# Optimization experiments

Measured on AMD Instinct MI355X. Metric: run time of the kernel, lower is better.

Reference implementation:

```python
import jax, jax.numpy as jnp
import numpy as np

B, C, N, M = 4096, 1024, 256, 64
EPS = 1e-8


def _linear_params(key, out_dim, in_dim):
    kw, kb = jax.random.split(key)
    lim = 1.0 / np.sqrt(in_dim)
    W = jax.random.uniform(kw, (out_dim, in_dim), jnp.float32, -lim, lim)
    b = jax.random.uniform(kb, (out_dim,), jnp.float32, -lim, lim)
    return W, b


def setup_inputs() -> dict:
    key = jax.random.key(0)
    ks = jax.random.split(key, 10)
    emb = jax.random.normal(ks[0], (B, C), jnp.float32)
    w_prev = jax.random.uniform(ks[1], (B, N), jnp.float32)
    w_prev = w_prev / jnp.sum(w_prev, axis=1, keepdims=True)  # valid weighting
    memory = jax.random.normal(ks[2], (B, N, M), jnp.float32) * 0.1
    Wk, bk = _linear_params(ks[3], M, C)
    Wbeta, bbeta = _linear_params(ks[4], 1, C)
    Wg, bg = _linear_params(ks[5], 1, C)
    Ws, bs = _linear_params(ks[6], 3, C)
    Wgamma, bgamma = _linear_params(ks[7], 1, C)
    We, be = _linear_params(ks[8], M, C)
    Wa, ba = _linear_params(ks[9], M, C)
    return {
        'embeddings': emb, 'w_prev': w_prev, 'memory': memory,
        'Wk': Wk, 'bk': bk, 'Wbeta': Wbeta, 'bbeta': bbeta,
        'Wg': Wg, 'bg': bg, 'Ws': Ws, 'bs': bs,
        'Wgamma': Wgamma, 'bgamma': bgamma,
        'We': We, 'be': be, 'Wa': Wa, 'ba': ba,
    }


def _forward(embeddings, w_prev, memory, Wk, bk, Wbeta, bbeta, Wg, bg,
             Ws, bs, Wgamma, bgamma, We, be, Wa, ba):
    k = embeddings @ Wk.T + bk                                  # [B, M]
    beta = jax.nn.softplus(embeddings @ Wbeta.T + bbeta)        # [B, 1]
    g = jax.nn.sigmoid(embeddings @ Wg.T + bg)                  # [B, 1]
    s = jax.nn.softmax(embeddings @ Ws.T + bs, axis=1)          # [B, 3]
    gamma = 1.0 + jax.nn.softplus(embeddings @ Wgamma.T + bgamma)  # [B, 1]
    e = jax.nn.sigmoid(embeddings @ We.T + be)                  # [B, M]
    a = embeddings @ Wa.T + ba                                  # [B, M]

    # content addressing: beta-scaled cosine similarity + softmax
    dot = jnp.einsum('bnm,bm->bn', memory, k)                   # [B, N]
    mem_norm = jnp.linalg.norm(memory, axis=-1)                 # [B, N]
    k_norm = jnp.linalg.norm(k, axis=-1, keepdims=True)         # [B, 1]
    cos = dot / (jnp.maximum(mem_norm, EPS) * jnp.maximum(k_norm, EPS))
    w_c = jax.nn.softmax(beta * cos, axis=1)                    # [B, N]

    # interpolation gate
    w_g = g * w_c + (1.0 - g) * w_prev                          # [B, N]

    # circular 3-tap shift: c[i] = s0*w[i-1] + s1*w[i] + s2*w[i+1]
    w_s = (s[:, 0:1] * jnp.roll(w_g, 1, axis=1)
           + s[:, 1:2] * w_g
           + s[:, 2:3] * jnp.roll(w_g, -1, axis=1))             # [B, N]

    # sharpen
    w_pow = jnp.power(w_s, gamma)                               # [B, N]
    w = w_pow / (jnp.sum(w_pow, axis=1, keepdims=True) + 1e-16)

    # erase / add write (outer products)
    erase = w[:, :, None] * e[:, None, :]                       # [B, N, M]
    add = w[:, :, None] * a[:, None, :]                         # [B, N, M]
    new_memory = memory * (1.0 - erase) + add
    return w, new_memory


def reference(embeddings, w_prev, memory, Wk, bk, Wbeta, bbeta, Wg, bg,
              Ws, bs, Wgamma, bgamma, We, be, Wa, ba):
    return _forward(embeddings, w_prev, memory, Wk, bk, Wbeta, bbeta,
                    Wg, bg, Ws, bs, Wgamma, bgamma, We, be, Wa, ba)
```

## Files before the change

kernel.cpp:

```cpp
#include <hip/hip_runtime.h>
#include <hip/hip_bf16.h>

#define B_DIM 4096
#define C_DIM 1024
#define N_DIM 256
#define M_DIM 64
#define GPAD  208
#define NG    198
#define EPSC  1e-8f
#define SMS   68

typedef __attribute__((ext_vector_type(8))) short bfrag_t;
typedef __attribute__((ext_vector_type(4))) float ffrag_t;

__device__ __forceinline__ short f2b(float f) {
    __hip_bfloat16 h = __float2bfloat16(f);
    return *reinterpret_cast<short*>(&h);
}
__device__ __forceinline__ float softplus_f(float x) {
    return fmaxf(x, 0.f) + log1pf(expf(-fabsf(x)));
}
__device__ __forceinline__ float sigmoid_f(float x) {
    return 1.f / (1.f + expf(-x));
}
__device__ __forceinline__ float warp_red_max(float v) {
#pragma unroll
    for (int off = 32; off; off >>= 1) v = fmaxf(v, __shfl_xor(v, off));
    return v;
}
__device__ __forceinline__ float warp_red_sum(float v) {
#pragma unroll
    for (int off = 32; off; off >>= 1) v += __shfl_xor(v, off);
    return v;
}

__global__ __launch_bounds__(256) void build_wcat(
    const float* __restrict__ Wk, const float* __restrict__ Wbeta,
    const float* __restrict__ Wg, const float* __restrict__ Ws,
    const float* __restrict__ Wgamma, const float* __restrict__ We,
    const float* __restrict__ Wa, short* __restrict__ wcat)
{
    int idx = blockIdx.x * 256 + threadIdx.x;
    if (idx >= GPAD * C_DIM) return;
    int n = idx >> 10, k = idx & (C_DIM - 1);
    float v;
    if (n < 64)        v = Wk[n * C_DIM + k];
    else if (n == 64)  v = Wbeta[k];
    else if (n == 65)  v = Wg[k];
    else if (n < 69)   v = Ws[(n - 66) * C_DIM + k];
    else if (n == 69)  v = Wgamma[k];
    else if (n < 134)  v = We[(n - 70) * C_DIM + k];
    else if (n < NG)   v = Wa[(n - 134) * C_DIM + k];
    else               v = 0.f;
    wcat[idx] = f2b(v);
}

__global__ __launch_bounds__(64) void gates_gemm(
    const float* __restrict__ emb,
    const short* __restrict__ wcat,
    float* __restrict__ gates)
{
    const int lane = threadIdx.x;
    const int row0 = blockIdx.x << 4;
    const int m    = lane & 15;
    const int ko   = (lane >> 4) << 3;

    const float* arow = emb + (size_t)(row0 + m) * C_DIM + ko;
    const short* brow = wcat + m * C_DIM + ko;

    ffrag_t acc[13];
#pragma unroll
    for (int t = 0; t < 13; ++t) acc[t] = (ffrag_t)(0.f);

    for (int k = 0; k < C_DIM; k += 32) {
        float4 a0 = *(const float4*)(arow + k);
        float4 a1 = *(const float4*)(arow + k + 4);
        bfrag_t af;
        af[0] = f2b(a0.x); af[1] = f2b(a0.y); af[2] = f2b(a0.z); af[3] = f2b(a0.w);
        af[4] = f2b(a1.x); af[5] = f2b(a1.y); af[6] = f2b(a1.z); af[7] = f2b(a1.w);
#pragma unroll
        for (int t = 0; t < 13; ++t) {
            bfrag_t bf = *(const bfrag_t*)(brow + t * (16 * C_DIM) + k);
            acc[t] = __builtin_amdgcn_mfma_f32_16x16x32_bf16(af, bf, acc[t], 0, 0, 0);
        }
    }

    const int crow = row0 + ((lane >> 4) << 2);
#pragma unroll
    for (int t = 0; t < 13; ++t) {
        int n = (t << 4) + m;
#pragma unroll
        for (int r = 0; r < 4; ++r)
            gates[(size_t)(crow + r) * GPAD + n] = acc[t][r];
    }
}

__global__ __launch_bounds__(256) void ntm_fused(
    const float* __restrict__ w_prev,
    const float* __restrict__ memory,
    const float* __restrict__ gates,
    const float* __restrict__ bk, const float* __restrict__ bbeta,
    const float* __restrict__ bg, const float* __restrict__ bs,
    const float* __restrict__ bgamma, const float* __restrict__ be,
    const float* __restrict__ ba,
    float* __restrict__ out_w,
    float* __restrict__ out_mem)
{
    const int b = blockIdx.x;
    const int t = threadIdx.x;

    __shared__ __align__(16) float sm[N_DIM * SMS];
    __shared__ __align__(16) float pre[GPAD];
    __shared__ __align__(16) float kvf[M_DIM];
    __shared__ __align__(16) float ev[M_DIM];
    __shared__ __align__(16) float av[M_DIM];
    __shared__ __align__(16) float wgs[N_DIM];
    __shared__ __align__(16) float wsh[N_DIM];
    __shared__ float scal[8];
    __shared__ float redA[4], redB[4], redC[4];

    float wprev_t = w_prev[(size_t)b * N_DIM + t];

    const float4* msrc = (const float4*)(memory + (size_t)b * (N_DIM * M_DIM));
#pragma unroll
    for (int i = 0; i < 16; ++i) {
        int q = t + (i << 8);
        float4 v = msrc[q];
        int n = q >> 4, c4 = q & 15;
        *(float4*)&sm[n * SMS + (c4 << 2)] = v;
    }
    if (t < GPAD) pre[t] = gates[(size_t)b * GPAD + t];
    __syncthreads();

    if (t < 64) {
        float kt = pre[t] + bk[t];
        kvf[t] = kt;
        ev[t]  = sigmoid_f(pre[70 + t] + be[t]);
        av[t]  = pre[134 + t] + ba[t];
        float sq = warp_red_sum(kt * kt);
        if (t == 0) scal[6] = sqrtf(sq);
    }
    if (t == 64) {
        scal[0] = softplus_f(pre[64] + bbeta[0]);
        scal[1] = sigmoid_f(pre[65] + bg[0]);
        float x0 = pre[66] + bs[0];
        float x1 = pre[67] + bs[1];
        float x2 = pre[68] + bs[2];
        float mx = fmaxf(x0, fmaxf(x1, x2));
        float e0 = expf(x0 - mx), e1 = expf(x1 - mx), e2 = expf(x2 - mx);
        float inv = 1.f / (e0 + e1 + e2);
        scal[3] = e0 * inv; scal[4] = e1 * inv; scal[5] = e2 * inv;
        scal[2] = 1.f + softplus_f(pre[69] + bgamma[0]);
    }
    __syncthreads();

    float dot = 0.f, nrm = 0.f;
    const float4* kv4 = (const float4*)kvf;
#pragma unroll
    for (int j = 0; j < 16; ++j) {
        float4 mv = *(const float4*)&sm[t * SMS + (j << 2)];
        float4 kj = kv4[j];
        dot = fmaf(mv.x, kj.x, dot); dot = fmaf(mv.y, kj.y, dot);
        dot = fmaf(mv.z, kj.z, dot); dot = fmaf(mv.w, kj.w, dot);
        nrm = fmaf(mv.x, mv.x, nrm); nrm = fmaf(mv.y, mv.y, nrm);
        nrm = fmaf(mv.z, mv.z, nrm); nrm = fmaf(mv.w, mv.w, nrm);
    }
    float cosv = dot / (fmaxf(sqrtf(nrm), EPSC) * fmaxf(scal[6], EPSC));
    float x = scal[0] * cosv;

    float mx = warp_red_max(x);
    if ((t & 63) == 0) redA[t >> 6] = mx;
    __syncthreads();
    mx = fmaxf(fmaxf(redA[0], redA[1]), fmaxf(redA[2], redA[3]));
    float ex = expf(x - mx);
    float sm_ = warp_red_sum(ex);
    if ((t & 63) == 0) redB[t >> 6] = sm_;
    __syncthreads();
    float wc = ex / (redB[0] + redB[1] + redB[2] + redB[3]);

    float g = scal[1];
    float wg = g * wc + (1.f - g) * wprev_t;
    wgs[t] = wg;
    __syncthreads();

    float ws_ = scal[3] * wgs[(t + 255) & 255] + scal[4] * wg + scal[5] * wgs[(t + 1) & 255];

    float wp = powf(fmaxf(ws_, 0.f), scal[2]);
    float ts = warp_red_sum(wp);
    if ((t & 63) == 0) redC[t >> 6] = ts;
    __syncthreads();
    float w = wp / (redC[0] + redC[1] + redC[2] + redC[3] + 1e-16f);

    out_w[(size_t)b * N_DIM + t] = w;
    wsh[t] = w;
    __syncthreads();

    float4* omem = (float4*)(out_mem + (size_t)b * (N_DIM * M_DIM));
    const float4* ev4 = (const float4*)ev;
    const float4* av4 = (const float4*)av;
#pragma unroll
    for (int i = 0; i < 16; ++i) {
        int q = t + (i << 8);
        int n = q >> 4, c4 = q & 15;
        float4 mv = *(const float4*)&sm[n * SMS + (c4 << 2)];
        float wn = wsh[n];
        float4 e4 = ev4[c4];
        float4 a4 = av4[c4];
        float4 r;
        r.x = fmaf(mv.x, -wn * e4.x, fmaf(wn, a4.x, mv.x));
        r.y = fmaf(mv.y, -wn * e4.y, fmaf(wn, a4.y, mv.y));
        r.z = fmaf(mv.z, -wn * e4.z, fmaf(wn, a4.z, mv.z));
        r.w = fmaf(mv.w, -wn * e4.w, fmaf(wn, a4.w, mv.w));
        omem[q] = r;
    }
}

extern "C" void kernel_launch(void* const* d_in, const int* in_sizes, int n_in,
                              void* d_out, int out_size, void* d_ws, size_t ws_size,
                              hipStream_t stream) {
    const float* emb    = (const float*)d_in[0];
    const float* w_prev = (const float*)d_in[1];
    const float* memory = (const float*)d_in[2];
    const float* Wk     = (const float*)d_in[3];
    const float* bk     = (const float*)d_in[4];
    const float* Wbeta  = (const float*)d_in[5];
    const float* bbeta  = (const float*)d_in[6];
    const float* Wg     = (const float*)d_in[7];
    const float* bg     = (const float*)d_in[8];
    const float* Ws     = (const float*)d_in[9];
    const float* bs     = (const float*)d_in[10];
    const float* Wgamma = (const float*)d_in[11];
    const float* bgamma = (const float*)d_in[12];
    const float* We     = (const float*)d_in[13];
    const float* be     = (const float*)d_in[14];
    const float* Wa     = (const float*)d_in[15];
    const float* ba     = (const float*)d_in[16];

    short* wcat  = (short*)d_ws;
    float* gates = (float*)((char*)d_ws + (size_t)GPAD * C_DIM * sizeof(short));

    float* out_w   = (float*)d_out;
    float* out_mem = out_w + (size_t)B_DIM * N_DIM;

    build_wcat<<<(GPAD * C_DIM + 255) / 256, 256, 0, stream>>>(
        Wk, Wbeta, Wg, Ws, Wgamma, We, Wa, wcat);
    gates_gemm<<<B_DIM / 16, 64, 0, stream>>>(emb, wcat, gates);
    ntm_fused<<<B_DIM, 256, 0, stream>>>(w_prev, memory, gates,
                                         bk, bbeta, bg, bs, bgamma, be, ba,
                                         out_w, out_mem);
}
```

Before: 587.1 us.

## Keep memory tile in registers and split gates GEMM across waves

```diff
diff --git a/kernel.cpp b/kernel.cpp
--- a/kernel.cpp
+++ b/kernel.cpp
@@ -8,7 +8,7 @@
 #define GPAD  208
 #define NG    198
 #define EPSC  1e-8f
-#define SMS   68
+#define PDS   17
 
 typedef __attribute__((ext_vector_type(8))) short bfrag_t;
 typedef __attribute__((ext_vector_type(4))) float ffrag_t;
@@ -55,47 +55,52 @@
     wcat[idx] = f2b(v);
 }
 
-__global__ __launch_bounds__(64) void gates_gemm(
-    const float* __restrict__ emb,
+__global__ __launch_bounds__(256) void cvt_emb(
+    const float* __restrict__ emb, short* __restrict__ embh)
+{
+    int idx = (blockIdx.x * 256 + threadIdx.x) << 3;
+    if (idx >= B_DIM * C_DIM) return;
+    float4 a0 = *(const float4*)(emb + idx);
+    float4 a1 = *(const float4*)(emb + idx + 4);
+    bfrag_t f;
+    f[0] = f2b(a0.x); f[1] = f2b(a0.y); f[2] = f2b(a0.z); f[3] = f2b(a0.w);
+    f[4] = f2b(a1.x); f[5] = f2b(a1.y); f[6] = f2b(a1.z); f[7] = f2b(a1.w);
+    *(bfrag_t*)(embh + idx) = f;
+}
+
+__global__ __launch_bounds__(256) void gates_gemm(
+    const short* __restrict__ embh,
     const short* __restrict__ wcat,
     float* __restrict__ gates)
 {
-    const int lane = threadIdx.x;
-    const int row0 = blockIdx.x << 4;
-    const int m    = lane & 15;
-    const int ko   = (lane >> 4) << 3;
-
-    const float* arow = emb + (size_t)(row0 + m) * C_DIM + ko;
-    const short* brow = wcat + m * C_DIM + ko;
-
-    ffrag_t acc[13];
-#pragma unroll
-    for (int t = 0; t < 13; ++t) acc[t] = (ffrag_t)(0.f);
-
+    const int wave = threadIdx.x >> 6;
+    const int lane = threadIdx.x & 63;
+    const int rg   = blockIdx.x >> 2;
+    const int tt   = ((blockIdx.x & 3) << 2) + wave;
+    if (tt >= 13) return;
+
+    const int m  = lane & 15;
+    const int ko = (lane >> 4) << 3;
+
+    const short* arow = embh + (size_t)(rg * 16 + m) * C_DIM + ko;
+    const short* brow = wcat + (size_t)(tt * 16 + m) * C_DIM + ko;
+
+    ffrag_t acc = (ffrag_t)(0.f);
+#pragma unroll 4
     for (int k = 0; k < C_DIM; k += 32) {
-        float4 a0 = *(const float4*)(arow + k);
-        float4 a1 = *(const float4*)(arow + k + 4);
-        bfrag_t af;
-        af[0] = f2b(a0.x); af[1] = f2b(a0.y); af[2] = f2b(a0.z); af[3] = f2b(a0.w);
-        af[4] = f2b(a1.x); af[5] = f2b(a1.y); af[6] = f2b(a1.z); af[7] = f2b(a1.w);
-#pragma unroll
-        for (int t = 0; t < 13; ++t) {
-            bfrag_t bf = *(const bfrag_t*)(brow + t * (16 * C_DIM) + k);
-            acc[t] = __builtin_amdgcn_mfma_f32_16x16x32_bf16(af, bf, acc[t], 0, 0, 0);
-        }
-    }
-
-    const int crow = row0 + ((lane >> 4) << 2);
-#pragma unroll
-    for (int t = 0; t < 13; ++t) {
-        int n = (t << 4) + m;
-#pragma unroll
-        for (int r = 0; r < 4; ++r)
-            gates[(size_t)(crow + r) * GPAD + n] = acc[t][r];
-    }
-}
-
-__global__ __launch_bounds__(256) void ntm_fused(
+        bfrag_t af = *(const bfrag_t*)(arow + k);
+        bfrag_t bf = *(const bfrag_t*)(brow + k);
+        acc = __builtin_amdgcn_mfma_f32_16x16x32_bf16(af, bf, acc, 0, 0, 0);
+    }
+
+    const int crow = rg * 16 + ((lane >> 4) << 2);
+    const int n = (tt << 4) + m;
+#pragma unroll
+    for (int rr = 0; rr < 4; ++rr)
+        gates[(size_t)(crow + rr) * GPAD + n] = acc[rr];
+}
+
+__global__ __launch_bounds__(256, 4) void ntm_fused(
     const float* __restrict__ w_prev,
     const float* __restrict__ memory,
     const float* __restrict__ gates,
@@ -108,28 +113,27 @@
 {
     const int b = blockIdx.x;
     const int t = threadIdx.x;
-
-    __shared__ __align__(16) float sm[N_DIM * SMS];
-    __shared__ __align__(16) float pre[GPAD];
+    const int r = t >> 4;
+    const int c = t & 15;
+
+    __shared__ __align__(16) float pdot[N_DIM * PDS];
+    __shared__ __align__(16) float pnrm[N_DIM * PDS];
+    __shared__ __align__(16) float pre[NG];
     __shared__ __align__(16) float kvf[M_DIM];
     __shared__ __align__(16) float ev[M_DIM];
     __shared__ __align__(16) float av[M_DIM];
-    __shared__ __align__(16) float wgs[N_DIM];
-    __shared__ __align__(16) float wsh[N_DIM];
+    __shared__ float wgs[N_DIM];
+    __shared__ float wsh[N_DIM];
     __shared__ float scal[8];
     __shared__ float redA[4], redB[4], redC[4];
 
+    const float4* msrc = (const float4*)(memory + (size_t)b * (N_DIM * M_DIM));
+    float4 v[16];
+#pragma unroll
+    for (int i = 0; i < 16; ++i) v[i] = msrc[t + (i << 8)];
+
     float wprev_t = w_prev[(size_t)b * N_DIM + t];
-
-    const float4* msrc = (const float4*)(memory + (size_t)b * (N_DIM * M_DIM));
-#pragma unroll
-    for (int i = 0; i < 16; ++i) {
-        int q = t + (i << 8);
-        float4 v = msrc[q];
-        int n = q >> 4, c4 = q & 15;
-        *(float4*)&sm[n * SMS + (c4 << 2)] = v;
-    }
-    if (t < GPAD) pre[t] = gates[(size_t)b * GPAD + t];
+    if (t < NG) pre[t] = gates[(size_t)b * GPAD + t];
     __syncthreads();
 
     if (t < 64) {
@@ -146,25 +150,35 @@
         float x0 = pre[66] + bs[0];
         float x1 = pre[67] + bs[1];
         float x2 = pre[68] + bs[2];
-        float mx = fmaxf(x0, fmaxf(x1, x2));
-        float e0 = expf(x0 - mx), e1 = expf(x1 - mx), e2 = expf(x2 - mx);
+        float mxs = fmaxf(x0, fmaxf(x1, x2));
+        float e0 = expf(x0 - mxs), e1 = expf(x1 - mxs), e2 = expf(x2 - mxs);
         float inv = 1.f / (e0 + e1 + e2);
         scal[3] = e0 * inv; scal[4] = e1 * inv; scal[5] = e2 * inv;
         scal[2] = 1.f + softplus_f(pre[69] + bgamma[0]);
     }
     __syncthreads();
 
+    float4 kc = *(const float4*)&kvf[c << 2];
+#pragma unroll
+    for (int i = 0; i < 16; ++i) {
+        float d, q;
+        d = v[i].x * kc.x;          q = v[i].x * v[i].x;
+        d = fmaf(v[i].y, kc.y, d);  q = fmaf(v[i].y, v[i].y, q);
+        d = fmaf(v[i].z, kc.z, d);  q = fmaf(v[i].z, v[i].z, q);
+        d = fmaf(v[i].w, kc.w, d);  q = fmaf(v[i].w, v[i].w, q);
+        int n = r + (i << 4);
+        pdot[n * PDS + c] = d;
+        pnrm[n * PDS + c] = q;
+    }
+    __syncthreads();
+
     float dot = 0.f, nrm = 0.f;
-    const float4* kv4 = (const float4*)kvf;
 #pragma unroll
     for (int j = 0; j < 16; ++j) {
-        float4 mv = *(const float4*)&sm[t * SMS + (j << 2)];
-        float4 kj = kv4[j];
-        dot = fmaf(mv.x, kj.x, dot); dot = fmaf(mv.y, kj.y, dot);
-        dot = fmaf(mv.z, kj.z, dot); dot = fmaf(mv.w, kj.w, dot);
-        nrm = fmaf(mv.x, mv.x, nrm); nrm = fmaf(mv.y, mv.y, nrm);
-        nrm = fmaf(mv.z, mv.z, nrm); nrm = fmaf(mv.w, mv.w, nrm);
-    }
+        dot += pdot[t * PDS + j];
+        nrm += pnrm[t * PDS + j];
+    }
+
     float cosv = dot / (fmaxf(sqrtf(nrm), EPSC) * fmaxf(scal[6], EPSC));
     float x = scal[0] * cosv;
 
@@ -196,22 +210,18 @@
     __syncthreads();
 
     float4* omem = (float4*)(out_mem + (size_t)b * (N_DIM * M_DIM));
-    const float4* ev4 = (const float4*)ev;
-    const float4* av4 = (const float4*)av;
+    float4 e4 = *(const float4*)&ev[c << 2];
+    float4 a4 = *(const float4*)&av[c << 2];
 #pragma unroll
     for (int i = 0; i < 16; ++i) {
-        int q = t + (i << 8);
-        int n = q >> 4, c4 = q & 15;
-        float4 mv = *(const float4*)&sm[n * SMS + (c4 << 2)];
-        float wn = wsh[n];
-        float4 e4 = ev4[c4];
-        float4 a4 = av4[c4];
-        float4 r;
-        r.x = fmaf(mv.x, -wn * e4.x, fmaf(wn, a4.x, mv.x));
-        r.y = fmaf(mv.y, -wn * e4.y, fmaf(wn, a4.y, mv.y));
-        r.z = fmaf(mv.z, -wn * e4.z, fmaf(wn, a4.z, mv.z));
-        r.w = fmaf(mv.w, -wn * e4.w, fmaf(wn, a4.w, mv.w));
-        omem[q] = r;
+        float wn = wsh[r + (i << 4)];
+        float4 m_ = v[i];
+        float4 rr;
+        rr.x = fmaf(m_.x, -wn * e4.x, fmaf(wn, a4.x, m_.x));
+        rr.y = fmaf(m_.y, -wn * e4.y, fmaf(wn, a4.y, m_.y));
+        rr.z = fmaf(m_.z, -wn * e4.z, fmaf(wn, a4.z, m_.z));
+        rr.w = fmaf(m_.w, -wn * e4.w, fmaf(wn, a4.w, m_.w));
+        omem[t + (i << 8)] = rr;
     }
 }
 
@@ -236,15 +246,19 @@
     const float* Wa     = (const float*)d_in[15];
     const float* ba     = (const float*)d_in[16];
 
+    const size_t WCAT_BYTES = (size_t)GPAD * C_DIM * sizeof(short);
+    const size_t EMBH_BYTES = (size_t)B_DIM * C_DIM * sizeof(short);
     short* wcat  = (short*)d_ws;
-    float* gates = (float*)((char*)d_ws + (size_t)GPAD * C_DIM * sizeof(short));
+    short* embh  = (short*)((char*)d_ws + WCAT_BYTES);
+    float* gates = (float*)((char*)d_ws + WCAT_BYTES + EMBH_BYTES);
 
     float* out_w   = (float*)d_out;
     float* out_mem = out_w + (size_t)B_DIM * N_DIM;
 
     build_wcat<<<(GPAD * C_DIM + 255) / 256, 256, 0, stream>>>(
         Wk, Wbeta, Wg, Ws, Wgamma, We, Wa, wcat);
-    gates_gemm<<<B_DIM / 16, 64, 0, stream>>>(emb, wcat, gates);
+    cvt_emb<<<(B_DIM * C_DIM / 8 + 255) / 256, 256, 0, stream>>>(emb, embh);
+    gates_gemm<<<(B_DIM / 16) * 4, 256, 0, stream>>>(embh, wcat, gates);
     ntm_fused<<<B_DIM, 256, 0, stream>>>(w_prev, memory, gates,
                                          bk, bbeta, bg, bs, bgamma, be, ba,
                                          out_w, out_mem);
```

Result: faster. 521.1 us (-11.2%).
